# Optimization experiments

Hardware: AMD Instinct MI355X
Metric: run time of the kernel (lower is better)

Reference implementation:

```python
import jax, jax.numpy as jnp
import numpy as np

NUM_POINTS = 17
T_MAX = 2.0

def _quadrature():
    t = jnp.linspace(0.0, T_MAX, NUM_POINTS + 1)[1:]            # (P,)
    dt = T_MAX / NUM_POINTS
    w = jnp.full((NUM_POINTS,), dt).at[0].set(dt / 2).at[-1].set(dt / 2)
    return t, w

def setup_inputs() -> dict:
    key = jax.random.key(0)
    x = jax.random.normal(key, (8388608,), dtype=jnp.float32)
    return {"x": x}

def reference(x) -> jnp.ndarray:
    t, w = _quadrature()
    # standardize (torch.std is unbiased, ddof=1)
    mu = x.mean()
    sd = x.std(ddof=1)
    xs = (x - mu) / (sd + 1e-8)
    # outer product of frequencies and samples: (P, N)
    tx = t[:, None] * xs[None, :]
    ecf_real = jnp.cos(tx).mean(axis=1)                         # (P,)
    ecf_imag = jnp.sin(tx).mean(axis=1)                         # (P,)
    ecf_sq = ecf_real ** 2 + ecf_imag ** 2
    tcf = jnp.exp(-0.5 * t ** 2)                                # theoretical CF of N(0,1)
    integrand = ecf_sq - 2.0 * ecf_real * tcf + tcf ** 2
    return jnp.sum(w * integrand)
```

## Files before the change

### kernel.cpp

```cpp
#include <hip/hip_runtime.h>
#include <math.h>

#define NFREQ 17
#define TPB 256
#define STAT_BLOCKS 1024
#define ECF_BLOCKS 1024
#define SPAD (2 * STAT_BLOCKS)

typedef float v2f __attribute__((ext_vector_type(2)));

#if __has_builtin(__builtin_elementwise_fma)
static __device__ __forceinline__ v2f v2fma(v2f a, v2f b, v2f c) {
    return __builtin_elementwise_fma(a, b, c);
}
#else
static __device__ __forceinline__ v2f v2fma(v2f a, v2f b, v2f c) {
    v2f r; r.x = __builtin_fmaf(a.x, b.x, c.x); r.y = __builtin_fmaf(a.y, b.y, c.y); return r;
}
#endif

__global__ void __launch_bounds__(TPB) stat_kernel(const float* __restrict__ x, long long n,
                                                   double* __restrict__ ws) {
    long long tid = blockIdx.x * (long long)blockDim.x + threadIdx.x;
    long long stride = (long long)gridDim.x * blockDim.x;
    long long n4 = n >> 2;
    const float4* x4 = (const float4*)x;
    double s = 0.0, s2 = 0.0;
    for (long long i = tid; i < n4; i += stride) {
        float4 v = x4[i];
        double a = v.x, b = v.y, c = v.z, d = v.w;
        s += (a + b) + (c + d);
        s2 += (a * a + b * b) + (c * c + d * d);
    }
    if (tid == 0) {
        for (long long i = n4 << 2; i < n; ++i) { double a = x[i]; s += a; s2 += a * a; }
    }
    for (int off = 32; off > 0; off >>= 1) { s += __shfl_down(s, off); s2 += __shfl_down(s2, off); }
    __shared__ double ls[4], ls2[4];
    int lane = threadIdx.x & 63, wid = threadIdx.x >> 6;
    if (lane == 0) { ls[wid] = s; ls2[wid] = s2; }
    __syncthreads();
    if (threadIdx.x == 0) {
        ws[2 * blockIdx.x + 0] = ls[0] + ls[1] + ls[2] + ls[3];
        ws[2 * blockIdx.x + 1] = ls2[0] + ls2[1] + ls2[2] + ls2[3];
    }
}

__global__ void __launch_bounds__(TPB) ecf_kernel(const float* __restrict__ x, long long n,
                                                  double* __restrict__ ws) {
    __shared__ double rls[4], rls2[4];
    __shared__ float sh_mu, sh_scale;
    {
        double s = 0.0, s2 = 0.0;
        for (int i = threadIdx.x; i < STAT_BLOCKS; i += TPB) { s += ws[2 * i]; s2 += ws[2 * i + 1]; }
        for (int off = 32; off > 0; off >>= 1) { s += __shfl_down(s, off); s2 += __shfl_down(s2, off); }
        int lane = threadIdx.x & 63, wid = threadIdx.x >> 6;
        if (lane == 0) { rls[wid] = s; rls2[wid] = s2; }
        __syncthreads();
        if (threadIdx.x == 0) {
            double S = rls[0] + rls[1] + rls[2] + rls[3];
            double S2 = rls2[0] + rls2[1] + rls2[2] + rls2[3];
            double mu_d = S / (double)n;
            double var = (S2 - (double)n * mu_d * mu_d) / (double)(n - 1);
            sh_mu = (float)mu_d;
            sh_scale = (float)((2.0 / 17.0) / (sqrt(var) + 1e-8));
        }
        __syncthreads();
    }
    const float muf = sh_mu, scale = sh_scale;
    const float nmus = -muf * scale;

    v2f acc[NFREQ];
#pragma unroll
    for (int p = 0; p < NFREQ; ++p) { acc[p].x = 0.f; acc[p].y = 0.f; }

    const float S1c = -1.6666654611e-1f, S2c = 8.3321608736e-3f, S3c = -1.9515295891e-4f;
    const float C2c = 4.166664568298827e-2f, C3c = -1.388731625493765e-3f,
                C4c = 2.443315711809948e-5f;

    auto proc = [&](float e) {
        float th = __builtin_fmaf(e, scale, nmus);
        float z = th * th;
        v2f zv; zv.x = z; zv.y = z;
        v2f A;  A.x = S3c; A.y = C4c;
        v2f B1; B1.x = S2c; B1.y = C3c;
        v2f B0; B0.x = S1c; B0.y = C2c;
        A = v2fma(zv, A, B1);
        A = v2fma(zv, A, B0);
        float s1 = __builtin_fmaf(th * z, A.x, th);
        float c1 = __builtin_fmaf(z, __builtin_fmaf(z, A.y, -0.5f), 1.0f);
        float two_c1 = c1 + c1;
        float c2 = __builtin_fmaf(two_c1, c1, -1.0f);
        float s2 = two_c1 * s1;
        float k2 = c2 + c2;
        v2f k2v; k2v.x = k2; k2v.y = k2;
        v2f f1;  f1.x = c1;  f1.y = s1;
        v2f f2;  f2.x = c2;  f2.y = s2;
        v2f mo1 = f1;
        v2f mo2; mo2.x = c1; mo2.y = -s1;
        v2f me1 = f2;
        v2f me2; me2.x = 1.0f; me2.y = 0.0f;
        acc[0] += f1;
        acc[1] += f2;
#pragma unroll
        for (int st = 1; st <= 8; ++st) {
            v2f fo = v2fma(k2v, mo1, -mo2);
            acc[2 * st] += fo;
            mo2 = mo1; mo1 = fo;
            if (st <= 7) {
                v2f fe = v2fma(k2v, me1, -me2);
                acc[2 * st + 1] += fe;
                me2 = me1; me1 = fe;
            }
        }
    };

    long long tid = blockIdx.x * (long long)blockDim.x + threadIdx.x;
    long long stride = (long long)ECF_BLOCKS * TPB;
    long long n4 = n >> 2;
    const float4* x4 = (const float4*)x;
    long long nfull = n4 / stride;
    long long k = 0;
    for (; k + 1 < nfull; k += 2) {
        float4 va = x4[tid + k * stride];
        float4 vb = x4[tid + (k + 1) * stride];
        proc(va.x); proc(va.y); proc(va.z); proc(va.w);
        proc(vb.x); proc(vb.y); proc(vb.z); proc(vb.w);
    }
    for (; k < nfull; ++k) {
        float4 v = x4[tid + k * stride];
        proc(v.x); proc(v.y); proc(v.z); proc(v.w);
    }
    for (long long idx = tid + nfull * stride; idx < n4; idx += stride) {
        float4 v = x4[idx];
        proc(v.x); proc(v.y); proc(v.z); proc(v.w);
    }
    if (tid == 0) {
        for (long long i = n4 << 2; i < n; ++i) proc(x[i]);
    }

#pragma unroll
    for (int p = 0; p < NFREQ; ++p) {
        float cx = acc[p].x, sy = acc[p].y;
        for (int off = 32; off > 0; off >>= 1) {
            cx += __shfl_down(cx, off);
            sy += __shfl_down(sy, off);
        }
        acc[p].x = cx; acc[p].y = sy;
    }
    __shared__ float lc[4][NFREQ], lsn[4][NFREQ];
    int lane = threadIdx.x & 63, wid = threadIdx.x >> 6;
    if (lane == 0) {
#pragma unroll
        for (int p = 0; p < NFREQ; ++p) { lc[wid][p] = acc[p].x; lsn[wid][p] = acc[p].y; }
    }
    __syncthreads();
    if (threadIdx.x < 2 * NFREQ) {
        int j = threadIdx.x;
        double v;
        if (j < NFREQ) v = (double)lc[0][j] + (double)lc[1][j] + (double)lc[2][j] + (double)lc[3][j];
        else { int p = j - NFREQ; v = (double)lsn[0][p] + (double)lsn[1][p] + (double)lsn[2][p] + (double)lsn[3][p]; }
        ws[SPAD + (long long)blockIdx.x * (2 * NFREQ) + j] = v;
    }
}

__global__ void __launch_bounds__(1024) finalize_kernel(const double* __restrict__ ws,
                                                        float* __restrict__ out, long long n) {
    const int J = 2 * NFREQ;
    const int SEG = 1024 / J;
    __shared__ double red[2 * NFREQ][30];
    __shared__ double sums[2 * NFREQ];
    int t = threadIdx.x;
    if (t < J * SEG) {
        int j = t % J, seg = t / J;
        const double* P = ws + SPAD;
        double a = 0.0, b = 0.0;
        int bi = seg;
        for (; bi + SEG < ECF_BLOCKS; bi += 2 * SEG) {
            a += P[(long long)bi * J + j];
            b += P[(long long)(bi + SEG) * J + j];
        }
        for (; bi < ECF_BLOCKS; bi += SEG) a += P[(long long)bi * J + j];
        red[j][seg] = a + b;
    }
    __syncthreads();
    if (t < J) {
        double s = 0.0;
        for (int g = 0; g < SEG; ++g) s += red[t][g];
        sums[t] = s;
    }
    __syncthreads();
    if (t == 0) {
        double nd = (double)n, dt = 2.0 / 17.0, total = 0.0;
        for (int k = 1; k <= NFREQ; ++k) {
            double tt = 2.0 * (double)k / 17.0;
            double r  = sums[k - 1] / nd;
            double im = sums[NFREQ + k - 1] / nd;
            double tcf = exp(-0.5 * tt * tt);
            double integrand = r * r + im * im - 2.0 * r * tcf + tcf * tcf;
            double w = (k == 1 || k == NFREQ) ? dt * 0.5 : dt;
            total += w * integrand;
        }
        out[0] = (float)total;
    }
}

extern "C" void kernel_launch(void* const* d_in, const int* in_sizes, int n_in,
                              void* d_out, int out_size, void* d_ws, size_t ws_size,
                              hipStream_t stream) {
    const float* x = (const float*)d_in[0];
    long long n = (long long)in_sizes[0];
    double* ws = (double*)d_ws;
    float* out = (float*)d_out;

    stat_kernel<<<STAT_BLOCKS, TPB, 0, stream>>>(x, n, ws);
    ecf_kernel<<<ECF_BLOCKS, TPB, 0, stream>>>(x, n, ws);
    finalize_kernel<<<1, 1024, 0, stream>>>(ws, out, n);
}
```

Measured before the change: 38.74 us.

## Fold cross-block reductions into last-block-done epilogues and use DPP wave sums

Removes the separate finalize kernel. Each of the two main kernels now uses an atomic counter so that the last block to finish performs the grid-wide reduction: stat computes mu and scale once, and ecf computes the final integral. The ecf kernel also replaces the shuffle-based wave reduction with DPP row operations, reading the result from lane 63. This trades a kernel launch and the redundant per-block stat reduction for atomics, threadfences and a memset node that resets the counters.

```diff
diff --git a/kernel.cpp b/kernel.cpp
--- a/kernel.cpp
+++ b/kernel.cpp
@@ -5,7 +5,9 @@
 #define TPB 256
 #define STAT_BLOCKS 1024
 #define ECF_BLOCKS 1024
-#define SPAD (2 * STAT_BLOCKS)
+
+#define D_STAT 8
+#define D_ECF  (D_STAT + 2 * STAT_BLOCKS)
 
 typedef float v2f __attribute__((ext_vector_type(2)));
 
@@ -19,8 +21,27 @@
 }
 #endif
 
-__global__ void __launch_bounds__(TPB) stat_kernel(const float* __restrict__ x, long long n,
-                                                   double* __restrict__ ws) {
+static __device__ __forceinline__ float dpp_sum64(float x) {
+    int v;
+    v = __builtin_amdgcn_update_dpp(0, __float_as_int(x), 0x111, 0xf, 0xf, false);
+    x += __int_as_float(v);
+    v = __builtin_amdgcn_update_dpp(0, __float_as_int(x), 0x112, 0xf, 0xf, false);
+    x += __int_as_float(v);
+    v = __builtin_amdgcn_update_dpp(0, __float_as_int(x), 0x114, 0xf, 0xf, false);
+    x += __int_as_float(v);
+    v = __builtin_amdgcn_update_dpp(0, __float_as_int(x), 0x118, 0xf, 0xf, false);
+    x += __int_as_float(v);
+    v = __builtin_amdgcn_update_dpp(0, __float_as_int(x), 0x142, 0xf, 0xf, false);
+    x += __int_as_float(v);
+    v = __builtin_amdgcn_update_dpp(0, __float_as_int(x), 0x143, 0xf, 0xf, false);
+    x += __int_as_float(v);
+    return x;
+}
+
+__global__ void __launch_bounds__(TPB) ep_stat(const float* __restrict__ x, long long n,
+                                               double* __restrict__ ws) {
+    int* ctr = (int*)ws;
+    float* musc = (float*)ws + 4;
     long long tid = blockIdx.x * (long long)blockDim.x + threadIdx.x;
     long long stride = (long long)gridDim.x * blockDim.x;
     long long n4 = n >> 2;
@@ -37,37 +58,46 @@
     }
     for (int off = 32; off > 0; off >>= 1) { s += __shfl_down(s, off); s2 += __shfl_down(s2, off); }
     __shared__ double ls[4], ls2[4];
+    __shared__ int amLast;
     int lane = threadIdx.x & 63, wid = threadIdx.x >> 6;
     if (lane == 0) { ls[wid] = s; ls2[wid] = s2; }
     __syncthreads();
     if (threadIdx.x == 0) {
-        ws[2 * blockIdx.x + 0] = ls[0] + ls[1] + ls[2] + ls[3];
-        ws[2 * blockIdx.x + 1] = ls2[0] + ls2[1] + ls2[2] + ls2[3];
-    }
-}
-
-__global__ void __launch_bounds__(TPB) ecf_kernel(const float* __restrict__ x, long long n,
-                                                  double* __restrict__ ws) {
-    __shared__ double rls[4], rls2[4];
-    __shared__ float sh_mu, sh_scale;
-    {
-        double s = 0.0, s2 = 0.0;
-        for (int i = threadIdx.x; i < STAT_BLOCKS; i += TPB) { s += ws[2 * i]; s2 += ws[2 * i + 1]; }
-        for (int off = 32; off > 0; off >>= 1) { s += __shfl_down(s, off); s2 += __shfl_down(s2, off); }
-        int lane = threadIdx.x & 63, wid = threadIdx.x >> 6;
-        if (lane == 0) { rls[wid] = s; rls2[wid] = s2; }
+        ws[D_STAT + 2 * blockIdx.x + 0] = ls[0] + ls[1] + ls[2] + ls[3];
+        ws[D_STAT + 2 * blockIdx.x + 1] = ls2[0] + ls2[1] + ls2[2] + ls2[3];
+        __threadfence();
+        amLast = (atomicAdd(&ctr[0], 1) == STAT_BLOCKS - 1);
+    }
+    __syncthreads();
+    if (amLast) {
+        __threadfence();
+        double ps = 0.0, ps2 = 0.0;
+        for (int i = threadIdx.x; i < STAT_BLOCKS; i += TPB) {
+            ps  += ws[D_STAT + 2 * i];
+            ps2 += ws[D_STAT + 2 * i + 1];
+        }
+        for (int off = 32; off > 0; off >>= 1) {
+            ps  += __shfl_down(ps, off);
+            ps2 += __shfl_down(ps2, off);
+        }
+        if (lane == 0) { ls[wid] = ps; ls2[wid] = ps2; }
         __syncthreads();
         if (threadIdx.x == 0) {
-            double S = rls[0] + rls[1] + rls[2] + rls[3];
-            double S2 = rls2[0] + rls2[1] + rls2[2] + rls2[3];
+            double S  = ls[0] + ls[1] + ls[2] + ls[3];
+            double S2 = ls2[0] + ls2[1] + ls2[2] + ls2[3];
             double mu_d = S / (double)n;
             double var = (S2 - (double)n * mu_d * mu_d) / (double)(n - 1);
-            sh_mu = (float)mu_d;
-            sh_scale = (float)((2.0 / 17.0) / (sqrt(var) + 1e-8));
-        }
-        __syncthreads();
-    }
-    const float muf = sh_mu, scale = sh_scale;
+            musc[0] = (float)mu_d;
+            musc[1] = (float)((2.0 / 17.0) / (sqrt(var) + 1e-8));
+        }
+    }
+}
+
+__global__ void __launch_bounds__(TPB) ep_ecf(const float* __restrict__ x, long long n,
+                                              double* __restrict__ ws, float* __restrict__ out) {
+    int* ctr = (int*)ws;
+    const float muf = ((const float*)ws)[4];
+    const float scale = ((const float*)ws)[5];
     const float nmus = -muf * scale;
 
     v2f acc[NFREQ];
@@ -141,67 +171,63 @@
 
 #pragma unroll
     for (int p = 0; p < NFREQ; ++p) {
-        float cx = acc[p].x, sy = acc[p].y;
-        for (int off = 32; off > 0; off >>= 1) {
-            cx += __shfl_down(cx, off);
-            sy += __shfl_down(sy, off);
-        }
-        acc[p].x = cx; acc[p].y = sy;
+        acc[p].x = dpp_sum64(acc[p].x);
+        acc[p].y = dpp_sum64(acc[p].y);
     }
     __shared__ float lc[4][NFREQ], lsn[4][NFREQ];
+    __shared__ int amLast;
     int lane = threadIdx.x & 63, wid = threadIdx.x >> 6;
-    if (lane == 0) {
+    if (lane == 63) {
 #pragma unroll
         for (int p = 0; p < NFREQ; ++p) { lc[wid][p] = acc[p].x; lsn[wid][p] = acc[p].y; }
     }
     __syncthreads();
-    if (threadIdx.x < 2 * NFREQ) {
-        int j = threadIdx.x;
+    int t = threadIdx.x;
+    if (t < 2 * NFREQ) {
+        int j = t;
         double v;
         if (j < NFREQ) v = (double)lc[0][j] + (double)lc[1][j] + (double)lc[2][j] + (double)lc[3][j];
         else { int p = j - NFREQ; v = (double)lsn[0][p] + (double)lsn[1][p] + (double)lsn[2][p] + (double)lsn[3][p]; }
-        ws[SPAD + (long long)blockIdx.x * (2 * NFREQ) + j] = v;
-    }
-}
-
-__global__ void __launch_bounds__(1024) finalize_kernel(const double* __restrict__ ws,
-                                                        float* __restrict__ out, long long n) {
-    const int J = 2 * NFREQ;
-    const int SEG = 1024 / J;
-    __shared__ double red[2 * NFREQ][30];
-    __shared__ double sums[2 * NFREQ];
-    int t = threadIdx.x;
-    if (t < J * SEG) {
-        int j = t % J, seg = t / J;
-        const double* P = ws + SPAD;
-        double a = 0.0, b = 0.0;
-        int bi = seg;
-        for (; bi + SEG < ECF_BLOCKS; bi += 2 * SEG) {
-            a += P[(long long)bi * J + j];
-            b += P[(long long)(bi + SEG) * J + j];
-        }
-        for (; bi < ECF_BLOCKS; bi += SEG) a += P[(long long)bi * J + j];
-        red[j][seg] = a + b;
-    }
-    __syncthreads();
-    if (t < J) {
-        double s = 0.0;
-        for (int g = 0; g < SEG; ++g) s += red[t][g];
-        sums[t] = s;
-    }
-    __syncthreads();
-    if (t == 0) {
-        double nd = (double)n, dt = 2.0 / 17.0, total = 0.0;
-        for (int k = 1; k <= NFREQ; ++k) {
-            double tt = 2.0 * (double)k / 17.0;
-            double r  = sums[k - 1] / nd;
-            double im = sums[NFREQ + k - 1] / nd;
-            double tcf = exp(-0.5 * tt * tt);
-            double integrand = r * r + im * im - 2.0 * r * tcf + tcf * tcf;
-            double w = (k == 1 || k == NFREQ) ? dt * 0.5 : dt;
-            total += w * integrand;
-        }
-        out[0] = (float)total;
+        ws[D_ECF + (long long)blockIdx.x * (2 * NFREQ) + j] = v;
+    }
+    __threadfence();
+    __syncthreads();
+    if (t == 0) amLast = (atomicAdd(&ctr[1], 1) == ECF_BLOCKS - 1);
+    __syncthreads();
+
+    if (amLast) {
+        __threadfence();
+        const int J = 2 * NFREQ;
+        const int SEG = 7;
+        __shared__ double red[2 * NFREQ][SEG];
+        __shared__ double sums[2 * NFREQ];
+        if (t < J * SEG) {
+            int j = t % J, seg = t / J;
+            const double* P = ws + D_ECF;
+            double a = 0.0;
+            for (int b = seg; b < ECF_BLOCKS; b += SEG) a += P[(long long)b * J + j];
+            red[j][seg] = a;
+        }
+        __syncthreads();
+        if (t < J) {
+            double ssum = 0.0;
+            for (int g = 0; g < SEG; ++g) ssum += red[t][g];
+            sums[t] = ssum;
+        }
+        __syncthreads();
+        if (t == 0) {
+            double nd = (double)n, dt = 2.0 / 17.0, total = 0.0;
+            for (int kk = 1; kk <= NFREQ; ++kk) {
+                double tt = 2.0 * (double)kk / 17.0;
+                double r  = sums[kk - 1] / nd;
+                double im = sums[NFREQ + kk - 1] / nd;
+                double tcf = exp(-0.5 * tt * tt);
+                double integrand = r * r + im * im - 2.0 * r * tcf + tcf * tcf;
+                double w = (kk == 1 || kk == NFREQ) ? dt * 0.5 : dt;
+                total += w * integrand;
+            }
+            out[0] = (float)total;
+        }
     }
 }
 
@@ -213,7 +239,7 @@
     double* ws = (double*)d_ws;
     float* out = (float*)d_out;
 
-    stat_kernel<<<STAT_BLOCKS, TPB, 0, stream>>>(x, n, ws);
-    ecf_kernel<<<ECF_BLOCKS, TPB, 0, stream>>>(x, n, ws);
-    finalize_kernel<<<1, 1024, 0, stream>>>(ws, out, n);
-}
+    hipMemsetAsync(d_ws, 0, 16, stream);
+    ep_stat<<<STAT_BLOCKS, TPB, 0, stream>>>(x, n, ws);
+    ep_ecf<<<ECF_BLOCKS, TPB, 0, stream>>>(x, n, ws, out);
+}
```

Result: slower. 149.2 us (+285.0%).
